# Kernel optimization log

Hardware: AMD Instinct MI355X
Metric: run time of the kernel (lower is better)

Reference implementation:

```python
import jax, jax.numpy as jnp
import numpy as np
import math

HEAD_DIM = 64
NQ = 24          # num query heads
NKV = 4          # num kv heads
HIDDEN = 1536
WINDOW = 256     # sliding window (layer_idx=0 -> active)
THETA = 10000.0
EPS = 1e-6


def _rope(x, cos, sin):
    # x: [B,S,H,D]; cos/sin: [S,1,D//2]  (broadcast over B and heads)
    xr = x.reshape(*x.shape[:-1], -1, 2)
    x1, x2 = xr[..., 0], xr[..., 1]
    r = jnp.stack([x1 * cos - x2 * sin, x2 * cos + x1 * sin], axis=-1)
    return r.reshape(x.shape)


def setup_inputs() -> dict:
    key = jax.random.key(0)
    k1, k2, k3 = jax.random.split(key, 3)
    B, S = 2, 2048
    x = jax.random.normal(k1, (B, S, HIDDEN), dtype=jnp.float32)
    norm_scale = jnp.ones((HIDDEN,), dtype=jnp.float32)             # RMSNorm scale
    w_qkv = jax.random.normal(k2, ((NQ + 2 * NKV) * HEAD_DIM, HIDDEN), dtype=jnp.float32) * 0.02
    w_out = jax.random.normal(k3, (HIDDEN, NQ * HEAD_DIM), dtype=jnp.float32) * 0.02
    return {"x": x, "norm_scale": norm_scale, "w_qkv": w_qkv, "w_out": w_out, "start_pos": 0}


def reference(x, norm_scale, w_qkv, w_out, start_pos):
    B, S, _ = x.shape
    # RMSNorm
    var = jnp.mean(x * x, axis=-1, keepdims=True)
    xn = x * jax.lax.rsqrt(var + EPS) * norm_scale
    # QKV projection (nn.Linear: x @ W^T)
    qkv = xn @ w_qkv.T
    qs, kvs = NQ * HEAD_DIM, NKV * HEAD_DIM
    q = qkv[..., :qs].reshape(B, S, NQ, HEAD_DIM)
    k = qkv[..., qs:qs + kvs].reshape(B, S, NKV, HEAD_DIM)
    v = qkv[..., qs + kvs:].reshape(B, S, NKV, HEAD_DIM)
    # RoPE
    inv_freq = 1.0 / (THETA ** (jnp.arange(0, HEAD_DIM, 2, dtype=jnp.float32) / HEAD_DIM))
    t = jnp.arange(start_pos, start_pos + S, dtype=jnp.float32)
    freqs = t[:, None] * inv_freq[None, :]                       # [S, D//2]
    cos, sin = jnp.cos(freqs)[:, None, :], jnp.sin(freqs)[:, None, :]
    q = _rope(q, cos, sin)
    k = _rope(k, cos, sin)
    # GQA: expand kv heads (repeat_interleave over head dim)
    rep = NQ // NKV
    k = jnp.repeat(k, rep, axis=2)
    v = jnp.repeat(v, rep, axis=2)
    # attention with causal + sliding-window mask
    scale = 1.0 / math.sqrt(HEAD_DIM)
    scores = jnp.einsum('bqhd,bkhd->bhqk', q * scale, k)        # [B,H,S,S]
    ipos = start_pos + jnp.arange(S)
    j = jnp.arange(S)
    mask = (j[None, :] > ipos[:, None]) | (j[None, :] < ipos[:, None] - WINDOW)
    scores = jnp.where(mask[None, None], -jnp.inf, scores)
    probs = jax.nn.softmax(scores, axis=-1)
    attn = jnp.einsum('bhqk,bkhd->bqhd', probs, v).reshape(B, S, NQ * HEAD_DIM)
    # output projection + residual
    return x + attn @ w_out.T
```

## Files before the change

### kernel.cpp

```cpp
#include <hip/hip_runtime.h>
#include <hip/hip_bf16.h>

typedef float f32x4 __attribute__((ext_vector_type(4)));
typedef short s16x8 __attribute__((ext_vector_type(8)));
typedef unsigned short u16;

#define B_ 2
#define S_ 2048
#define HID 1536
#define NQ_ 24
#define NKV_ 4
#define HD 64
#define NTOK (B_*S_)
#define QKVN ((NQ_+2*NKV_)*HD)
#define ROPE_BLOCKS ((NTOK*28*32)/256)
#define VT_BLOCKS (B_*NKV_*(S_/64))

#define LDS_FENCE() asm volatile("" ::: "memory")

__device__ __forceinline__ float bf2f(u16 u) {
  unsigned int x = ((unsigned int)u) << 16;
  float f; __builtin_memcpy(&f, &x, 4); return f;
}
__device__ __forceinline__ u16 f2bf(float f) {
  unsigned int u; __builtin_memcpy(&u, &f, 4);
  u += 0x7fffu + ((u >> 16) & 1u);
  return (u16)(u >> 16);
}
__device__ __forceinline__ unsigned long long pk4bf(float a, float b, float c, float d) {
  __hip_bfloat162 x = __float22bfloat162_rn(make_float2(a, b));
  __hip_bfloat162 y = __float22bfloat162_rn(make_float2(c, d));
  unsigned int xi, yi;
  __builtin_memcpy(&xi, &x, 4);
  __builtin_memcpy(&yi, &y, 4);
  return (unsigned long long)xi | ((unsigned long long)yi << 32);
}

__global__ __launch_bounds__(256) void k_cvt2(const float* __restrict__ s0, int n0q,
                                              const float* __restrict__ s1, int n1q,
                                              u16* __restrict__ dst) {
  int i = blockIdx.x * 256 + threadIdx.x;
  if (i >= n0q + n1q) return;
  const float* src = (i < n0q) ? s0 : s1;
  int j = (i < n0q) ? i : i - n0q;
  f32x4 v = ((const f32x4*)src)[j];
  *(unsigned long long*)(dst + (size_t)i*4) = pk4bf(v[0], v[1], v[2], v[3]);
}

__global__ __launch_bounds__(384) void k_rmsnorm(const float* __restrict__ x,
                                                 const float* __restrict__ g,
                                                 u16* __restrict__ xn) {
  int row = blockIdx.x;
  int t = threadIdx.x;
  f32x4 v = ((const f32x4*)(x + (size_t)row * HID))[t];
  float ss = v[0]*v[0] + v[1]*v[1] + v[2]*v[2] + v[3]*v[3];
#pragma unroll
  for (int off = 1; off < 64; off <<= 1) ss += __shfl_xor(ss, off);
  __shared__ float red[6];
  if ((t & 63) == 0) red[t >> 6] = ss;
  __syncthreads();
  float tot = red[0] + red[1] + red[2] + red[3] + red[4] + red[5];
  float rs = rsqrtf(tot * (1.f/HID) + 1e-6f);
  f32x4 gv = ((const f32x4*)g)[t];
  ((unsigned long long*)(xn + (size_t)row * HID))[t] =
      pk4bf(v[0]*rs*gv[0], v[1]*rs*gv[1], v[2]*rs*gv[2], v[3]*rs*gv[3]);
}

template <bool F32OUT>
__global__ __launch_bounds__(256) void k_gemm_bt(const u16* __restrict__ A,
                                                 const u16* __restrict__ W,
                                                 void* __restrict__ Cv,
                                                 const float* __restrict__ resid,
                                                 int N, int K) {
  __shared__ __align__(16) u16 As[2][128*32];
  __shared__ __align__(16) u16 Bs[2][128*32];
  int lin = blockIdx.x;
  int xcd = lin & 7, loc = lin >> 3;
  int mloc = loc & 3, nloc = loc >> 2;
  int m0 = (xcd*4 + mloc) * 128, n0 = nloc * 128;
  int tid = threadIdx.x;
  int w = tid >> 6, l = tid & 63;
  int wr = w >> 1, wc = w & 1;
  int c = l & 15, g = l >> 4;
  f32x4 acc[4][4] = {};
  const u16* Ag = A + (size_t)(m0 + w*32 + (l>>2))*K + (l&3)*8;
  const u16* Wg = W + (size_t)(n0 + w*32 + (l>>2))*K + (l&3)*8;
  const int woff = w*32*32;
  for (int k0 = 0; k0 < K; k0 += 64) {
#pragma unroll
    for (int hf = 0; hf < 2; hf++) {
      int kk = k0 + hf*32;
      __builtin_amdgcn_global_load_lds((const __attribute__((address_space(1))) void*)(Ag + kk),
                                       (__attribute__((address_space(3))) void*)(As[hf] + woff), 16, 0, 0);
      __builtin_amdgcn_global_load_lds((const __attribute__((address_space(1))) void*)(Ag + kk + (size_t)16*K),
                                       (__attribute__((address_space(3))) void*)(As[hf] + woff + 16*32), 16, 0, 0);
      __builtin_amdgcn_global_load_lds((const __attribute__((address_space(1))) void*)(Wg + kk),
                                       (__attribute__((address_space(3))) void*)(Bs[hf] + woff), 16, 0, 0);
      __builtin_amdgcn_global_load_lds((const __attribute__((address_space(1))) void*)(Wg + kk + (size_t)16*K),
                                       (__attribute__((address_space(3))) void*)(Bs[hf] + woff + 16*32), 16, 0, 0);
    }
    __syncthreads();
#pragma unroll
    for (int hf = 0; hf < 2; hf++) {
      s16x8 af[4], bq[4];
#pragma unroll
      for (int mt = 0; mt < 4; mt++) af[mt] = *(const s16x8*)(As[hf] + (wr*64 + mt*16 + c)*32 + g*8);
#pragma unroll
      for (int nt = 0; nt < 4; nt++) bq[nt] = *(const s16x8*)(Bs[hf] + (wc*64 + nt*16 + c)*32 + g*8);
#pragma unroll
      for (int mt = 0; mt < 4; mt++)
#pragma unroll
        for (int nt = 0; nt < 4; nt++)
          acc[mt][nt] = __builtin_amdgcn_mfma_f32_16x16x32_bf16(af[mt], bq[nt], acc[mt][nt], 0, 0, 0);
    }
    __syncthreads();
  }
#pragma unroll
  for (int mt = 0; mt < 4; mt++)
#pragma unroll
    for (int nt = 0; nt < 4; nt++)
#pragma unroll
      for (int r = 0; r < 4; r++) {
        int m = m0 + wr*64 + mt*16 + g*4 + r;
        int n = n0 + wc*64 + nt*16 + c;
        size_t off = (size_t)m*N + n;
        float vv = acc[mt][nt][r];
        if (F32OUT) {
          ((float*)Cv)[off] = vv + resid[off];
        } else {
          ((u16*)Cv)[off] = f2bf(vv);
        }
      }
}

__global__ __launch_bounds__(256) void k_rope_vt(const u16* __restrict__ qkv,
                                                 u16* __restrict__ q,
                                                 u16* __restrict__ k,
                                                 u16* __restrict__ vt,
                                                 const int* __restrict__ spp) {
  __shared__ u16 tile[64][65];
  int bid = blockIdx.x;
  if (bid < ROPE_BLOCKS) {
    int idx = bid * 256 + threadIdx.x;
    int p = idx & 31;
    int h = (idx >> 5) % 28;
    int tok = idx / 896;
    int s = tok & (S_ - 1);
    int b = tok >> 11;
    float t = (float)(spp[0] + s);
    float inv = powf(10000.f, -(float)p * (1.f/32.f));
    float fr = t * inv;
    float sn, cs;
    sincosf(fr, &sn, &cs);
    int col = (h < NQ_) ? h*64 + 2*p : HID + (h - NQ_)*64 + 2*p;
    unsigned int pr = *(const unsigned int*)(qkv + (size_t)tok*QKVN + col);
    float x1 = bf2f((u16)(pr & 0xffff));
    float x2 = bf2f((u16)(pr >> 16));
    float y1 = x1*cs - x2*sn;
    float y2 = x2*cs + x1*sn;
    unsigned int outp = (unsigned int)f2bf(y1) | ((unsigned int)f2bf(y2) << 16);
    if (h < NQ_) {
      *(unsigned int*)(q + (((size_t)(b*NQ_ + h))*S_ + s)*64 + 2*p) = outp;
    } else {
      *(unsigned int*)(k + (((size_t)(b*NKV_ + (h - NQ_)))*S_ + s)*64 + 2*p) = outp;
    }
  } else {
    int blk = bid - ROPE_BLOCKS;
    int st = blk & 31;
    int hk = (blk >> 5) & 3;
    int b = blk >> 7;
    int s0 = st * 64;
#pragma unroll
    for (int i = 0; i < 16; i++) {
      int ii = threadIdx.x + i*256;
      int r = ii >> 6, cc = ii & 63;
      tile[r][cc] = qkv[((size_t)(b*S_) + s0 + r)*QKVN + (NQ_+NKV_)*64 + hk*64 + cc];
    }
    __syncthreads();
#pragma unroll
    for (int i = 0; i < 16; i++) {
      int ii = threadIdx.x + i*256;
      int d = ii >> 6, s = ii & 63;
      vt[((size_t)(b*NKV_ + hk)*64 + d)*S_ + s0 + s] = tile[s][d];
    }
  }
}

__global__ __launch_bounds__(64, 3) void k_attn(const u16* __restrict__ q,
                                                const u16* __restrict__ k,
                                                const u16* __restrict__ vt,
                                                u16* __restrict__ ao,
                                                const int* __restrict__ spp) {
  __shared__ __align__(16) u16 Pt[32*72];
  int blk = blockIdx.x;
  int qb = blk & 63;
  int rest = blk >> 6;
  int h = rest % NQ_;
  int b = rest / NQ_;
  int q0 = qb * 32;
  int hk = h / (NQ_/NKV_);
  int l = threadIdx.x;
  int c = l & 15, g = l >> 4;
  int sp = spp[0];
  const u16* qptr = q + ((size_t)(b*NQ_ + h))*S_*64;
  const u16* kptr = k + ((size_t)(b*NKV_ + hk))*S_*64;
  const u16* vptr = vt + ((size_t)(b*NKV_ + hk))*64*S_;

  s16x8 qf[2][2];
#pragma unroll
  for (int qt = 0; qt < 2; qt++)
#pragma unroll
    for (int ks = 0; ks < 2; ks++)
      qf[qt][ks] = *(const s16x8*)(qptr + (size_t)(q0 + qt*16 + c)*64 + ks*32 + g*8);

  f32x4 o[4][2] = {};
  float m_run[2], l_run[2];
#pragma unroll
  for (int i = 0; i < 2; i++) { m_run[i] = -1e30f; l_run[i] = 0.f; }

  int lo = sp + q0 - 256; if (lo < 0) lo = 0;
  int hi = sp + q0 + 31;  if (hi > S_ - 1) hi = S_ - 1;
  int kt0 = lo >> 6, kt1 = hi >> 6;

  s16x8 kf[4][2];
#pragma unroll
  for (int km = 0; km < 4; km++)
#pragma unroll
    for (int ks = 0; ks < 2; ks++)
      kf[km][ks] = *(const s16x8*)(kptr + (size_t)(kt0*64 + km*16 + c)*64 + ks*32 + g*8);

  for (int kt = kt0; kt <= kt1; kt++) {
    f32x4 sa[4][2];
#pragma unroll
    for (int km = 0; km < 4; km++)
#pragma unroll
      for (int qt = 0; qt < 2; qt++) {
        f32x4 z = {};
        z = __builtin_amdgcn_mfma_f32_16x16x32_bf16(kf[km][0], qf[qt][0], z, 0, 0, 0);
        sa[km][qt] = __builtin_amdgcn_mfma_f32_16x16x32_bf16(kf[km][1], qf[qt][1], z, 0, 0, 0);
      }
    s16x8 vf[2][4];
#pragma unroll
    for (int ks = 0; ks < 2; ks++)
#pragma unroll
      for (int dt = 0; dt < 4; dt++)
        vf[ks][dt] = *(const s16x8*)(vptr + (size_t)(dt*16 + c)*S_ + kt*64 + ks*32 + g*8);

    bool full = (kt*64 + 63 <= sp + q0) && (kt*64 >= sp + q0 - 225);
#pragma unroll
    for (int qt = 0; qt < 2; qt++) {
      float mx = -1e30f;
      if (full) {
#pragma unroll
        for (int km = 0; km < 4; km++)
#pragma unroll
          for (int r = 0; r < 4; r++) {
            float sv = sa[km][qt][r] * 0.125f;
            sa[km][qt][r] = sv;
            mx = fmaxf(mx, sv);
          }
      } else {
        int pos = sp + q0 + qt*16 + c;
#pragma unroll
        for (int km = 0; km < 4; km++)
#pragma unroll
          for (int r = 0; r < 4; r++) {
            int key = kt*64 + km*16 + g*4 + r;
            float sv = sa[km][qt][r] * 0.125f;
            sv = ((unsigned)(pos - key) <= 256u) ? sv : -1e30f;
            sa[km][qt][r] = sv;
            mx = fmaxf(mx, sv);
          }
      }
      mx = fmaxf(mx, __shfl_xor(mx, 16));
      mx = fmaxf(mx, __shfl_xor(mx, 32));
      float mnew = fmaxf(m_run[qt], mx);
      float alpha = __expf(m_run[qt] - mnew);
      m_run[qt] = mnew;
      float rsum = 0.f;
#pragma unroll
      for (int km = 0; km < 4; km++) {
        float p0 = __expf(sa[km][qt][0] - mnew);
        float p1 = __expf(sa[km][qt][1] - mnew);
        float p2 = __expf(sa[km][qt][2] - mnew);
        float p3 = __expf(sa[km][qt][3] - mnew);
        rsum += p0 + p1 + p2 + p3;
        *(unsigned long long*)(Pt + (qt*16 + c)*72 + km*16 + g*4) = pk4bf(p0, p1, p2, p3);
      }
      rsum += __shfl_xor(rsum, 16);
      rsum += __shfl_xor(rsum, 32);
      l_run[qt] = l_run[qt]*alpha + rsum;
#pragma unroll
      for (int dt = 0; dt < 4; dt++) {
        o[dt][qt][0] *= alpha; o[dt][qt][1] *= alpha;
        o[dt][qt][2] *= alpha; o[dt][qt][3] *= alpha;
      }
    }
    if (kt < kt1) {
#pragma unroll
      for (int km = 0; km < 4; km++)
#pragma unroll
        for (int ks = 0; ks < 2; ks++)
          kf[km][ks] = *(const s16x8*)(kptr + (size_t)((kt+1)*64 + km*16 + c)*64 + ks*32 + g*8);
    }
    LDS_FENCE();
#pragma unroll
    for (int ks = 0; ks < 2; ks++)
#pragma unroll
      for (int qt = 0; qt < 2; qt++) {
        s16x8 pf = *(const s16x8*)(Pt + (qt*16 + c)*72 + ks*32 + g*8);
#pragma unroll
        for (int dt = 0; dt < 4; dt++)
          o[dt][qt] = __builtin_amdgcn_mfma_f32_16x16x32_bf16(vf[ks][dt], pf, o[dt][qt], 0, 0, 0);
      }
    LDS_FENCE();
  }
#pragma unroll
  for (int qt = 0; qt < 2; qt++) {
    float inv = 1.f / l_run[qt];
    int qi = q0 + qt*16 + c;
    u16* row = ao + ((size_t)(b*S_) + qi)*HID + h*64;
#pragma unroll
    for (int dt = 0; dt < 4; dt++)
      *(unsigned long long*)(row + dt*16 + g*4) =
          pk4bf(o[dt][qt][0]*inv, o[dt][qt][1]*inv, o[dt][qt][2]*inv, o[dt][qt][3]*inv);
  }
}

extern "C" void kernel_launch(void* const* d_in, const int* in_sizes, int n_in,
                              void* d_out, int out_size, void* d_ws, size_t ws_size,
                              hipStream_t stream) {
  const float* x_f32    = (const float*)d_in[0];
  const float* g_f32    = (const float*)d_in[1];
  const float* wqkv_f32 = (const float*)d_in[2];
  const float* wout_f32 = (const float*)d_in[3];
  const int*   spp      = (const int*)d_in[4];
  char* ws = (char*)d_ws;
  u16* wqkvb = (u16*)(ws);
  u16* woutb = (u16*)(ws + 6291456);
  u16* xn    = (u16*)(ws + 11010048);
  u16* qkv   = (u16*)(ws + 23592960);
  u16* qbuf  = (u16*)(ws + 40370176);
  u16* kbuf  = (u16*)(ws + 52953088);
  u16* vtb   = (u16*)(ws + 55050240);
  u16* attn  = xn;

  const int nwq4 = QKVN*HID/4, nwo4 = HID*HID/4;
  k_cvt2<<<(nwq4 + nwo4 + 255)/256, 256, 0, stream>>>(wqkv_f32, nwq4, wout_f32, nwo4, wqkvb);
  k_rmsnorm<<<NTOK, 384, 0, stream>>>(x_f32, g_f32, xn);
  k_gemm_bt<false><<<32*(QKVN/128), 256, 0, stream>>>(xn, wqkvb, qkv, nullptr, QKVN, HID);
  k_rope_vt<<<ROPE_BLOCKS + VT_BLOCKS, 256, 0, stream>>>(qkv, qbuf, kbuf, vtb, spp);
  k_attn<<<B_*NQ_*(S_/32), 64, 0, stream>>>(qbuf, kbuf, vtb, attn, spp);
  k_gemm_bt<true><<<32*(HID/128), 256, 0, stream>>>(attn, woutb, d_out, x_f32, HID, HID);
}
```

Before: 236.1 us.

## Interleave QK MFMA with softmax per q-tile, remap blocks per XCD, add setprio

The attention loop now computes QK scores one q-tile at a time, interleaving each tile's MFMAs with its softmax. V fragments are loaded first, and the next K tile is prefetched earlier, right after the second tile's MFMAs. MFMA sections are wrapped in s_setprio to favor matrix issue across waves. Block indices are remapped so each of the 8 XCDs handles a contiguous group of batch-head pairs to improve L2 reuse of K/V, and the RoPE frequency uses exp2f instead of powf. The intent is to cut register pressure and hide memory latency, at the risk of the compiler reordering loads less favorably.

```diff
diff --git a/kernel.cpp b/kernel.cpp
--- a/kernel.cpp
+++ b/kernel.cpp
@@ -148,7 +148,7 @@
     int s = tok & (S_ - 1);
     int b = tok >> 11;
     float t = (float)(spp[0] + s);
-    float inv = powf(10000.f, -(float)p * (1.f/32.f));
+    float inv = exp2f((float)p * -0.41524101186f);
     float fr = t * inv;
     float sn, cs;
     sincosf(fr, &sn, &cs);
@@ -192,11 +192,12 @@
                                                 u16* __restrict__ ao,
                                                 const int* __restrict__ spp) {
   __shared__ __align__(16) u16 Pt[32*72];
-  int blk = blockIdx.x;
-  int qb = blk & 63;
-  int rest = blk >> 6;
-  int h = rest % NQ_;
-  int b = rest / NQ_;
+  int lin = blockIdx.x;
+  int xcd = lin & 7, loc = lin >> 3;
+  int qb = loc & 63;
+  int bh = xcd * 6 + (loc >> 6);
+  int h = bh % NQ_;
+  int b = bh / NQ_;
   int q0 = qb * 32;
   int hk = h / (NQ_/NKV_);
   int l = threadIdx.x;
@@ -230,33 +231,40 @@
       kf[km][ks] = *(const s16x8*)(kptr + (size_t)(kt0*64 + km*16 + c)*64 + ks*32 + g*8);
 
   for (int kt = kt0; kt <= kt1; kt++) {
-    f32x4 sa[4][2];
-#pragma unroll
-    for (int km = 0; km < 4; km++)
-#pragma unroll
-      for (int qt = 0; qt < 2; qt++) {
+    s16x8 vf[2][4];
+#pragma unroll
+    for (int ks = 0; ks < 2; ks++)
+#pragma unroll
+      for (int dt = 0; dt < 4; dt++)
+        vf[ks][dt] = *(const s16x8*)(vptr + (size_t)(dt*16 + c)*S_ + kt*64 + ks*32 + g*8);
+
+    bool full = (kt*64 + 63 <= sp + q0) && (kt*64 >= sp + q0 - 225);
+#pragma unroll
+    for (int qt = 0; qt < 2; qt++) {
+      f32x4 sa[4];
+      __builtin_amdgcn_s_setprio(1);
+#pragma unroll
+      for (int km = 0; km < 4; km++) {
         f32x4 z = {};
         z = __builtin_amdgcn_mfma_f32_16x16x32_bf16(kf[km][0], qf[qt][0], z, 0, 0, 0);
-        sa[km][qt] = __builtin_amdgcn_mfma_f32_16x16x32_bf16(kf[km][1], qf[qt][1], z, 0, 0, 0);
-      }
-    s16x8 vf[2][4];
-#pragma unroll
-    for (int ks = 0; ks < 2; ks++)
-#pragma unroll
-      for (int dt = 0; dt < 4; dt++)
-        vf[ks][dt] = *(const s16x8*)(vptr + (size_t)(dt*16 + c)*S_ + kt*64 + ks*32 + g*8);
-
-    bool full = (kt*64 + 63 <= sp + q0) && (kt*64 >= sp + q0 - 225);
-#pragma unroll
-    for (int qt = 0; qt < 2; qt++) {
+        sa[km] = __builtin_amdgcn_mfma_f32_16x16x32_bf16(kf[km][1], qf[qt][1], z, 0, 0, 0);
+      }
+      __builtin_amdgcn_s_setprio(0);
+      if (qt == 1 && kt < kt1) {
+#pragma unroll
+        for (int km = 0; km < 4; km++)
+#pragma unroll
+          for (int ks = 0; ks < 2; ks++)
+            kf[km][ks] = *(const s16x8*)(kptr + (size_t)((kt+1)*64 + km*16 + c)*64 + ks*32 + g*8);
+      }
       float mx = -1e30f;
       if (full) {
 #pragma unroll
         for (int km = 0; km < 4; km++)
 #pragma unroll
           for (int r = 0; r < 4; r++) {
-            float sv = sa[km][qt][r] * 0.125f;
-            sa[km][qt][r] = sv;
+            float sv = sa[km][r] * 0.125f;
+            sa[km][r] = sv;
             mx = fmaxf(mx, sv);
           }
       } else {
@@ -266,9 +274,9 @@
 #pragma unroll
           for (int r = 0; r < 4; r++) {
             int key = kt*64 + km*16 + g*4 + r;
-            float sv = sa[km][qt][r] * 0.125f;
+            float sv = sa[km][r] * 0.125f;
             sv = ((unsigned)(pos - key) <= 256u) ? sv : -1e30f;
-            sa[km][qt][r] = sv;
+            sa[km][r] = sv;
             mx = fmaxf(mx, sv);
           }
       }
@@ -280,10 +288,10 @@
       float rsum = 0.f;
 #pragma unroll
       for (int km = 0; km < 4; km++) {
-        float p0 = __expf(sa[km][qt][0] - mnew);
-        float p1 = __expf(sa[km][qt][1] - mnew);
-        float p2 = __expf(sa[km][qt][2] - mnew);
-        float p3 = __expf(sa[km][qt][3] - mnew);
+        float p0 = __expf(sa[km][0] - mnew);
+        float p1 = __expf(sa[km][1] - mnew);
+        float p2 = __expf(sa[km][2] - mnew);
+        float p3 = __expf(sa[km][3] - mnew);
         rsum += p0 + p1 + p2 + p3;
         *(unsigned long long*)(Pt + (qt*16 + c)*72 + km*16 + g*4) = pk4bf(p0, p1, p2, p3);
       }
@@ -296,14 +304,8 @@
         o[dt][qt][2] *= alpha; o[dt][qt][3] *= alpha;
       }
     }
-    if (kt < kt1) {
-#pragma unroll
-      for (int km = 0; km < 4; km++)
-#pragma unroll
-        for (int ks = 0; ks < 2; ks++)
-          kf[km][ks] = *(const s16x8*)(kptr + (size_t)((kt+1)*64 + km*16 + c)*64 + ks*32 + g*8);
-    }
     LDS_FENCE();
+    __builtin_amdgcn_s_setprio(1);
 #pragma unroll
     for (int ks = 0; ks < 2; ks++)
 #pragma unroll
@@ -313,6 +315,7 @@
         for (int dt = 0; dt < 4; dt++)
           o[dt][qt] = __builtin_amdgcn_mfma_f32_16x16x32_bf16(vf[ks][dt], pf, o[dt][qt], 0, 0, 0);
       }
+    __builtin_amdgcn_s_setprio(0);
     LDS_FENCE();
   }
 #pragma unroll
```

Measured after the change: 221.9 us. -6.0%, faster.
